# Performance work log

Measured on AMD Instinct MI355X. Metric: run time of the kernel, lower is better.

## Reference

```python
import jax, jax.numpy as jnp
import numpy as np
from jax.scipy.special import erf

N_POINTS = 4096
N_EVENTS = 1000000
BETA = 1.0   # init_beta, constant (not a Parameter in the torch module)
ALPHA = 1.0  # torch.ones((1,1)) buffer
WEIGHT = 1.0


def setup_inputs() -> dict:
    key = jax.random.key(0)
    k1, k2, k3, k4, k5 = jax.random.split(key, 5)
    return {
        "z0": jax.random.uniform(k1, (N_POINTS, 2), dtype=jnp.float32),
        "v0": jax.random.uniform(k2, (N_POINTS, 2), dtype=jnp.float32),
        "event_times": jax.random.uniform(k3, (N_EVENTS,), dtype=jnp.float32),
        "t0": jnp.zeros((), dtype=jnp.float32),
        "tn": jnp.ones((), dtype=jnp.float32),
        "u_idx": jax.random.randint(k4, (N_EVENTS,), 0, N_POINTS, dtype=jnp.int64) if jax.config.read('jax_enable_x64') else jax.random.randint(k4, (N_EVENTS,), 0, N_POINTS).astype(jnp.int32),
        "v_idx": jax.random.randint(k5, (N_EVENTS,), 0, N_POINTS).astype(jnp.int32),
    }


def reference(z0, v0, event_times, t0, tn, u_idx, v_idx):
    beta = jnp.float32(BETA)
    alpha = jnp.float32(ALPHA)

    # ---- event term: sum_e beta - ||z_u(t_e) - z_v(t_e)||^2,  z(t) = z0 + v0*t (a0 == 0)
    dz0 = z0[u_idx] - z0[v_idx]                      # [E, 2]
    dv0 = v0[u_idx] - v0[v_idx]                      # [E, 2]
    dz = dz0 + dv0 * event_times[:, None]            # [E, 2]
    d2 = jnp.sum(dz * dz, axis=-1)                   # [E]
    event_intensity = jnp.sum(beta - d2)

    # ---- non-event term: analytic Hawkes integral over all triu pairs
    i, j = jnp.triu_indices(z0.shape[0], k=1)        # static, [P]
    a = z0[i, 0] - z0[j, 0]
    b = z0[i, 1] - z0[j, 1]
    m = v0[i, 0] - v0[j, 0]
    n = v0[i, 1] - v0[j, 1]
    mn2 = m * m + n * n                              # [P]
    s = jnp.sqrt(alpha * mn2)
    cross = a * n - b * m
    dot = a * m + b * n
    expo = jnp.exp((-(cross * cross) * alpha + mn2 * beta) / mn2)
    sqrt_pi = jnp.float32(np.sqrt(np.pi))
    integral = (-sqrt_pi * expo
                * (erf(alpha * (mn2 * t0 + dot) / s) - erf(alpha * (mn2 * tn + dot) / s))
                / (2.0 * s))                          # [P]
    non_event_intensity = jnp.sum(integral)

    return event_intensity - WEIGHT * non_event_intensity
```

## Files before the change

kernel.cpp:

```cpp
#include <hip/hip_runtime.h>

#define NPTS   4096
#define NEVT   1000000
#define NQUAD  (NEVT / 4)
#define TILE   64
#define NT     (NPTS / TILE)
#define PAIR_BLOCKS (NT * (NT + 1) / 2)
#define BLK    256
#define GRID   512

__device__ __forceinline__ float fast_erff(float x) {
    float ax = __builtin_fabsf(x);
    float t  = __builtin_amdgcn_rcpf(__builtin_fmaf(0.3275911f, ax, 1.0f));
    float p  = __builtin_fmaf(t, 1.061405429f, -1.453152027f);
    p = __builtin_fmaf(t, p, 1.421413741f);
    p = __builtin_fmaf(t, p, -0.284496736f);
    p = __builtin_fmaf(t, p, 0.254829592f);
    p = p * t;
    float e = __builtin_amdgcn_exp2f(-ax * ax * 1.4426950408889634f);
    float r = __builtin_fmaf(-p, e, 1.0f);
    return __builtin_copysignf(r, x);
}

__global__ __launch_bounds__(BLK) void hawkes_fused(
    const float* __restrict__ z0, const float* __restrict__ v0,
    const float* __restrict__ et, const float* __restrict__ t0p,
    const float* __restrict__ tnp, const int* __restrict__ uix,
    const int* __restrict__ vix, float* __restrict__ out)
{
    __shared__ float4 pts[NPTS];
    __shared__ float  red[BLK / 64];
    const int tid = threadIdx.x;
    const float2* z2 = (const float2*)z0;
    const float2* v2 = (const float2*)v0;

    #pragma unroll
    for (int k = 0; k < NPTS / BLK; ++k) {
        int p = tid + k * BLK;
        float2 zp = z2[p], vp = v2[p];
        pts[p] = make_float4(zp.x, zp.y, vp.x, vp.y);
    }
    __syncthreads();

    float acc_ev = 0.0f;
    {
        const int stride = GRID * BLK;
        for (int q = (int)blockIdx.x * BLK + tid; q < NQUAD; q += stride) {
            int base = q * 4;
            float4 t4 = *(const float4*)(et + base);
            int4   u4 = *(const int4*)(uix + base);
            int4   v4 = *(const int4*)(vix + base);
            float tt[4] = {t4.x, t4.y, t4.z, t4.w};
            int   uu[4] = {u4.x, u4.y, u4.z, u4.w};
            int   vv[4] = {v4.x, v4.y, v4.z, v4.w};
            #pragma unroll
            for (int e = 0; e < 4; ++e) {
                float4 P = pts[uu[e]];
                float4 Q = pts[vv[e]];
                float dx = __builtin_fmaf(P.z - Q.z, tt[e], P.x - Q.x);
                float dy = __builtin_fmaf(P.w - Q.w, tt[e], P.y - Q.y);
                acc_ev += 1.0f - (dx * dx + dy * dy);
            }
        }
    }

    const float t0 = *t0p;
    const float tn = *tnp;
    const int il = tid & 63;
    const int jw = tid >> 6;
    float acc_pr = 0.0f;
    for (int L = (int)blockIdx.x; L < PAIR_BLOCKS; L += GRID) {
        int bi = (int)((129.0f - sqrtf((float)(16641 - 8 * L))) * 0.5f);
        while (bi * NT - bi * (bi - 1) / 2 > L) --bi;
        while ((bi + 1) * NT - (bi + 1) * bi / 2 <= L) ++bi;
        int bj = bi + (L - (bi * NT - bi * (bi - 1) / 2));

        const int i = bi * TILE + il;
        float4 Pi = pts[i];
        #pragma unroll
        for (int k = 0; k < 16; ++k) {
            int jl = jw * 16 + k;
            int j  = bj * TILE + jl;
            if (j > i) {
                float4 tj = pts[j];
                float a = Pi.x - tj.x;
                float b = Pi.y - tj.y;
                float m = Pi.z - tj.z;
                float n = Pi.w - tj.w;
                float mn2   = __builtin_fmaf(m, m, n * n);
                float cross = __builtin_fmaf(a, n, -b * m);
                float dot   = __builtin_fmaf(a, m, b * n);
                float invs  = __builtin_amdgcn_rsqf(mn2);
                float rmn2  = invs * invs;
                float ex    = __builtin_fmaf(-cross * cross, rmn2, 1.0f);
                float expo  = __builtin_amdgcn_exp2f(ex * 1.4426950408889634f);
                float arg0  = __builtin_fmaf(mn2, t0, dot) * invs;
                float arg1  = __builtin_fmaf(mn2, tn, dot) * invs;
                float df    = fast_erff(arg1) - fast_erff(arg0);
                acc_pr = __builtin_fmaf(df * expo, invs, acc_pr);
            }
        }
    }

    float contrib = __builtin_fmaf(-0.8862269254527580f, acc_pr, acc_ev);

    #pragma unroll
    for (int off = 32; off > 0; off >>= 1)
        contrib += __shfl_down(contrib, off, 64);
    if ((tid & 63) == 0) red[tid >> 6] = contrib;
    __syncthreads();
    if (tid == 0) {
        float s = red[0] + red[1] + red[2] + red[3];
        atomicAdd(out, s);
    }
}

extern "C" void kernel_launch(void* const* d_in, const int* in_sizes, int n_in,
                              void* d_out, int out_size, void* d_ws, size_t ws_size,
                              hipStream_t stream) {
    const float* z0  = (const float*)d_in[0];
    const float* v0  = (const float*)d_in[1];
    const float* et  = (const float*)d_in[2];
    const float* t0p = (const float*)d_in[3];
    const float* tnp = (const float*)d_in[4];
    const int*   uix = (const int*)d_in[5];
    const int*   vix = (const int*)d_in[6];
    float* out = (float*)d_out;

    hipMemsetAsync(out, 0, sizeof(float), stream);
    hipLaunchKernelGGL(hawkes_fused, dim3(GRID), dim3(BLK), 0, stream,
                       z0, v0, et, t0p, tnp, uix, vix, out);
}
```

Before: 92.23 us.

## Balance pair-tile work evenly across waves and double block size

```diff
diff --git a/kernel.cpp b/kernel.cpp
--- a/kernel.cpp
+++ b/kernel.cpp
@@ -6,8 +6,12 @@
 #define TILE   64
 #define NT     (NPTS / TILE)
 #define PAIR_BLOCKS (NT * (NT + 1) / 2)
-#define BLK    256
+#define BLK    512
 #define GRID   512
+#define NWAVES (GRID * (BLK / 64))
+#define NUNITS (PAIR_BLOCKS * 64)
+#define PERW   (NUNITS / NWAVES)
+#define REMW   (NUNITS % NWAVES)
 
 __device__ __forceinline__ float fast_erff(float x) {
     float ax = __builtin_fabsf(x);
@@ -22,7 +26,7 @@
     return __builtin_copysignf(r, x);
 }
 
-__global__ __launch_bounds__(BLK) void hawkes_fused(
+__global__ __launch_bounds__(BLK, 4) void hawkes_fused(
     const float* __restrict__ z0, const float* __restrict__ v0,
     const float* __restrict__ et, const float* __restrict__ t0p,
     const float* __restrict__ tnp, const int* __restrict__ uix,
@@ -44,8 +48,8 @@
 
     float acc_ev = 0.0f;
     {
-        const int stride = GRID * BLK;
-        for (int q = (int)blockIdx.x * BLK + tid; q < NQUAD; q += stride) {
+        int q = (int)blockIdx.x * BLK + tid;
+        if (q < NQUAD) {
             int base = q * 4;
             float4 t4 = *(const float4*)(et + base);
             int4   u4 = *(const int4*)(uix + base);
@@ -66,39 +70,44 @@
 
     const float t0 = *t0p;
     const float tn = *tnp;
-    const int il = tid & 63;
-    const int jw = tid >> 6;
+    const int il  = tid & 63;
+    const int wid = (int)blockIdx.x * (BLK / 64) + (tid >> 6);
+    int n = PERW + (wid < REMW ? 1 : 0);
+    int u = wid * PERW + (wid < REMW ? wid : REMW);
+    int Lc = -1, ibase = 0, jbase = 0;
+    float4 Pi = make_float4(0.f, 0.f, 0.f, 0.f);
     float acc_pr = 0.0f;
-    for (int L = (int)blockIdx.x; L < PAIR_BLOCKS; L += GRID) {
-        int bi = (int)((129.0f - sqrtf((float)(16641 - 8 * L))) * 0.5f);
-        while (bi * NT - bi * (bi - 1) / 2 > L) --bi;
-        while ((bi + 1) * NT - (bi + 1) * bi / 2 <= L) ++bi;
-        int bj = bi + (L - (bi * NT - bi * (bi - 1) / 2));
-
-        const int i = bi * TILE + il;
-        float4 Pi = pts[i];
-        #pragma unroll
-        for (int k = 0; k < 16; ++k) {
-            int jl = jw * 16 + k;
-            int j  = bj * TILE + jl;
-            if (j > i) {
-                float4 tj = pts[j];
-                float a = Pi.x - tj.x;
-                float b = Pi.y - tj.y;
-                float m = Pi.z - tj.z;
-                float n = Pi.w - tj.w;
-                float mn2   = __builtin_fmaf(m, m, n * n);
-                float cross = __builtin_fmaf(a, n, -b * m);
-                float dot   = __builtin_fmaf(a, m, b * n);
-                float invs  = __builtin_amdgcn_rsqf(mn2);
-                float rmn2  = invs * invs;
-                float ex    = __builtin_fmaf(-cross * cross, rmn2, 1.0f);
-                float expo  = __builtin_amdgcn_exp2f(ex * 1.4426950408889634f);
-                float arg0  = __builtin_fmaf(mn2, t0, dot) * invs;
-                float arg1  = __builtin_fmaf(mn2, tn, dot) * invs;
-                float df    = fast_erff(arg1) - fast_erff(arg0);
-                acc_pr = __builtin_fmaf(df * expo, invs, acc_pr);
-            }
+    for (int s = 0; s < n; ++s, ++u) {
+        int L  = u >> 6;
+        int jl = u & 63;
+        if (L != Lc) {
+            int bi = (int)((129.0f - sqrtf((float)(16641 - 8 * L))) * 0.5f);
+            while (bi * NT - bi * (bi - 1) / 2 > L) --bi;
+            while ((bi + 1) * NT - (bi + 1) * bi / 2 <= L) ++bi;
+            int bj = bi + (L - (bi * NT - bi * (bi - 1) / 2));
+            ibase = bi * TILE; jbase = bj * TILE;
+            Pi = pts[ibase + il];
+            Lc = L;
+        }
+        int i = ibase + il;
+        int j = jbase + jl;
+        if (j > i) {
+            float4 tj = pts[j];
+            float a = Pi.x - tj.x;
+            float b = Pi.y - tj.y;
+            float m = Pi.z - tj.z;
+            float nn = Pi.w - tj.w;
+            float mn2   = __builtin_fmaf(m, m, nn * nn);
+            float cross = __builtin_fmaf(a, nn, -b * m);
+            float dot   = __builtin_fmaf(a, m, b * nn);
+            float invs  = __builtin_amdgcn_rsqf(mn2);
+            float rmn2  = invs * invs;
+            float ex    = __builtin_fmaf(-cross * cross, rmn2, 1.0f);
+            float expo  = __builtin_amdgcn_exp2f(ex * 1.4426950408889634f);
+            float arg0  = __builtin_fmaf(mn2, t0, dot) * invs;
+            float arg1  = __builtin_fmaf(mn2, tn, dot) * invs;
+            float df    = fast_erff(arg1) - fast_erff(arg0);
+            acc_pr = __builtin_fmaf(df * expo, invs, acc_pr);
         }
     }
 
@@ -110,7 +119,9 @@
     if ((tid & 63) == 0) red[tid >> 6] = contrib;
     __syncthreads();
     if (tid == 0) {
-        float s = red[0] + red[1] + red[2] + red[3];
+        float s = 0.0f;
+        #pragma unroll
+        for (int w = 0; w < BLK / 64; ++w) s += red[w];
         atomicAdd(out, s);
     }
 }
```

New measurement: 90.48 us. About the same (-1.9%).
